# Performance work log

Measured on AMD Instinct MI355X. Metric: run time of the kernel, lower is better.

The kernel has to match this reference:

```python
import jax, jax.numpy as jnp
import numpy as np

NUM_NODES = 50000
NUM_RELATIONS = 16
NUM_EDGES = 800000
HIDDEN = 64
NUM_CLASSES = 16


def setup_inputs() -> dict:
    key = jax.random.key(0)
    ks = jax.random.split(key, 8)
    edge_index = jax.random.randint(ks[0], (2, NUM_EDGES), 0, NUM_NODES, dtype=jnp.int32)
    edge_type = jax.random.randint(ks[1], (NUM_EDGES,), 0, NUM_RELATIONS, dtype=jnp.int32)
    node_emb = jax.random.normal(ks[2], (NUM_NODES, HIDDEN), dtype=jnp.float32) * 0.1
    W1 = jax.random.normal(ks[3], (NUM_RELATIONS, HIDDEN, HIDDEN), dtype=jnp.float32) * 0.1
    root1 = jax.random.normal(ks[4], (HIDDEN, HIDDEN), dtype=jnp.float32) * 0.1
    b1 = jnp.zeros((HIDDEN,), dtype=jnp.float32)
    W2 = jax.random.normal(ks[5], (NUM_RELATIONS, HIDDEN, NUM_CLASSES), dtype=jnp.float32) * 0.1
    root2 = jax.random.normal(ks[6], (HIDDEN, NUM_CLASSES), dtype=jnp.float32) * 0.1
    b2 = jnp.zeros((NUM_CLASSES,), dtype=jnp.float32)
    return {"edge_index": edge_index, "edge_type": edge_type, "node_emb": node_emb,
            "W1": W1, "root1": root1, "b1": b1, "W2": W2, "root2": root2, "b2": b2}


def rgcn_conv(x, src, dst, edge_type, W, root, bias, num_nodes):
    # PyG RGCNConv (aggr='mean', root_weight=True, bias=True, num_bases=None):
    # per relation r: transform all nodes, gather at src, scatter-MEAN at dst
    # (mean over edges of that relation per target node); sum over relations;
    # then add root transform and bias.
    out_dim = W.shape[-1]

    def body(acc, rw):
        W_r, r = rw
        h = x @ W_r                                   # [N, out]
        mask = (edge_type == r).astype(x.dtype)       # [E]
        msg = h[src] * mask[:, None]                  # [E, out]
        summed = jax.ops.segment_sum(msg, dst, num_segments=num_nodes)  # [N, out]
        cnt = jax.ops.segment_sum(mask, dst, num_segments=num_nodes)    # [N]
        mean = jnp.where(cnt[:, None] > 0, summed / jnp.maximum(cnt, 1.0)[:, None], 0.0)
        return acc + mean, None

    acc0 = jnp.zeros((num_nodes, out_dim), dtype=x.dtype)
    agg, _ = jax.lax.scan(body, acc0, (W, jnp.arange(W.shape[0])))
    return agg + x @ root + bias


def reference(edge_index, edge_type, node_emb, W1, root1, b1, W2, root2, b2):
    src, dst = edge_index[0], edge_index[1]
    n = node_emb.shape[0]
    x = rgcn_conv(node_emb, src, dst, edge_type, W1, root1, b1, n)
    x = jax.nn.relu(x)  # dropout p=0.0 -> identity
    x = rgcn_conv(x, src, dst, edge_type, W2, root2, b2, n)
    return x
```

## Files before the change

### kernel.cpp

```cpp
#include <hip/hip_runtime.h>
#include <hip/hip_bf16.h>

#define N_NODES 50000
#define NREL 16
#define HID 64
#define NCLS 16
#define NBKT (N_NODES * NREL)
#define SB 2048
#define NSB ((NBKT + SB - 1) / SB)
#define TILE 32
#define NTB ((N_NODES + TILE - 1) / TILE)
#define XCHUNKS (N_NODES * HID / 8)
#define W1N (17 * HID * HID)
#define W2N (17 * NCLS * HID)

typedef __attribute__((ext_vector_type(8))) short bf16x8;
typedef __attribute__((ext_vector_type(4))) float f32x4;

static __device__ __forceinline__ unsigned short f2bf(float f) {
    __hip_bfloat16 h = __float2bfloat16(f);
    return *reinterpret_cast<unsigned short*>(&h);
}
static __device__ __forceinline__ float bf2f(unsigned short u) {
    __hip_bfloat16 h;
    *reinterpret_cast<unsigned short*>(&h) = u;
    return __bfloat162float(h);
}


__global__ __launch_bounds__(256) void pre_k(const int* __restrict__ dstp,
                                             const int* __restrict__ et,
                                             int* __restrict__ bcnt,
                                             int* __restrict__ rank, int E,
                                             const float* __restrict__ x,
                                             const float* __restrict__ W1,
                                             const float* __restrict__ root1,
                                             const float* __restrict__ W2,
                                             const float* __restrict__ root2,
                                             ushort* __restrict__ xb,
                                             ushort* __restrict__ WbT1,
                                             ushort* __restrict__ WbT2) {
    int eb = (E + 255) >> 8;
    if ((int)blockIdx.x < eb) {
        int i = blockIdx.x * 256 + threadIdx.x;
        if (i < E) {
            int b = dstp[i] * NREL + et[i];
            rank[i] = atomicAdd(&bcnt[b], 1);
        }
        return;
    }
    int i = (blockIdx.x - eb) * 256 + threadIdx.x;
    if (i < XCHUNKS) {
        float4 f0 = *(const float4*)(x + (size_t)i * 8);
        float4 f1 = *(const float4*)(x + (size_t)i * 8 + 4);
        bf16x8 o;
        o[0] = (short)f2bf(f0.x); o[1] = (short)f2bf(f0.y);
        o[2] = (short)f2bf(f0.z); o[3] = (short)f2bf(f0.w);
        o[4] = (short)f2bf(f1.x); o[5] = (short)f2bf(f1.y);
        o[6] = (short)f2bf(f1.z); o[7] = (short)f2bf(f1.w);
        *(bf16x8*)(xb + (size_t)i * 8) = o;
    } else {
        int j = i - XCHUNKS;
        if (j < W1N) {
            int t = j >> 12, rem = j & 4095, n = rem >> 6, k = rem & 63;
            float v = (t < 16) ? W1[(size_t)t * HID * HID + k * HID + n]
                               : root1[k * HID + n];
            WbT1[j] = f2bf(v);
        } else {
            int m = j - W1N;
            if (m < W2N) {
                int t = m >> 10, rem = m & 1023, n = rem >> 6, k = rem & 63;
                float v = (t < 16) ? W2[(size_t)t * HID * NCLS + k * NCLS + n]
                                   : root2[k * NCLS + n];
                WbT2[m] = f2bf(v);
            }
        }
    }
}

__global__ __launch_bounds__(256) void scan1_k(const int* __restrict__ bcnt,
                                               int* __restrict__ bsum) {
    int b = blockIdx.x, t = threadIdx.x;
    int base = b * SB + t * 8;
    int s = 0;
#pragma unroll
    for (int j = 0; j < 8; ++j)
        if (base + j < NBKT) s += bcnt[base + j];
#pragma unroll
    for (int off = 1; off < 64; off <<= 1) s += __shfl_xor(s, off, 64);
    __shared__ int ws[4];
    if ((t & 63) == 0) ws[t >> 6] = s;
    __syncthreads();
    if (t == 0) bsum[b] = ws[0] + ws[1] + ws[2] + ws[3];
}

__global__ __launch_bounds__(512) void scan2_k(int* __restrict__ bsum,
                                               int* __restrict__ rstart, int E) {
    __shared__ int ts[512];
    int t = threadIdx.x;
    int v = (t < NSB) ? bsum[t] : 0;
    ts[t] = v;
    __syncthreads();
    int acc = v;
    for (int off = 1; off < 512; off <<= 1) {
        int u = (t >= off) ? ts[t - off] : 0;
        __syncthreads();
        acc += u;
        ts[t] = acc;
        __syncthreads();
    }
    if (t < NSB) bsum[t] = acc - v;
    if (t == 0) rstart[NBKT] = E;
}

__global__ __launch_bounds__(256) void scan3_k(int* __restrict__ bcnt,
                                               const int* __restrict__ bsum) {
    int b = blockIdx.x, t = threadIdx.x;
    int base = b * SB + t * 8;
    int a[8];
    int s = 0;
#pragma unroll
    for (int j = 0; j < 8; ++j) {
        a[j] = (base + j < NBKT) ? bcnt[base + j] : 0;
        s += a[j];
    }
    __shared__ int ts[256];
    ts[t] = s;
    __syncthreads();
    int acc = s;
    for (int off = 1; off < 256; off <<= 1) {
        int u = (t >= off) ? ts[t - off] : 0;
        __syncthreads();
        acc += u;
        ts[t] = acc;
        __syncthreads();
    }
    int run = bsum[b] + (acc - s);
#pragma unroll
    for (int j = 0; j < 8; ++j) {
        if (base + j < NBKT) bcnt[base + j] = run;
        run += a[j];
    }
}

__global__ __launch_bounds__(256) void scat_k(const int* __restrict__ srcp,
                                              const int* __restrict__ dstp,
                                              const int* __restrict__ et,
                                              const int* __restrict__ rank,
                                              const int* __restrict__ rstart,
                                              int2* __restrict__ sedge, int E) {
    int i = blockIdx.x * 256 + threadIdx.x;
    if (i < E) {
        int r = et[i];
        int b = dstp[i] * NREL + r;
        int lo = rstart[b], hi = rstart[b + 1];
        float inv = 1.0f / (float)(hi - lo);
        sedge[lo + rank[i]] = make_int2(srcp[i] | (r << 16), __float_as_int(inv));
    }
}


#define GFLUSH()                                                              \
    {                                                                         \
        bf16x8 o_;                                                            \
        o_[0] = (short)f2bf(acc[0]); o_[1] = (short)f2bf(acc[1]);             \
        o_[2] = (short)f2bf(acc[2]); o_[3] = (short)f2bf(acc[3]);             \
        o_[4] = (short)f2bf(acc[4]); o_[5] = (short)f2bf(acc[5]);             \
        o_[6] = (short)f2bf(acc[6]); o_[7] = (short)f2bf(acc[7]);             \
        *(bf16x8*)(Ab + ((curRel * (TILE * 128) + rowoff) ^ sw)) = o_;        \
        acc[0] = 0.f; acc[1] = 0.f; acc[2] = 0.f; acc[3] = 0.f;               \
        acc[4] = 0.f; acc[5] = 0.f; acc[6] = 0.f; acc[7] = 0.f;               \
    }

static __device__ __forceinline__ void gather_tile(char* Ab,
                                                   const ushort* __restrict__ ft,
                                                   const int2* __restrict__ sedge,
                                                   const int* __restrict__ rstart,
                                                   int dst0, int tid) {
    int g = tid >> 3, l8 = tid & 7;
    int node = dst0 + g;
    bool valid = node < N_NODES;

    int lo = 0, hi = 0;
    if (valid) {
        lo = rstart[node * NREL];
        hi = rstart[node * NREL + NREL];
    }
    int deg = hi - lo;
    int base = (deg > 0) ? lo : 0;
    int last = (deg > 0) ? hi - 1 : 0;

    int sw = (g & 7) << 4;
    int rowoff = (g << 7) + (l8 << 4);
    const bf16x8 zz = {0, 0, 0, 0, 0, 0, 0, 0};

    int2 d[32];
#pragma unroll
    for (int j = 0; j < 32; ++j) {
        int idx = base + j;
        if (idx > last) idx = last;
        d[j] = sedge[idx];
    }

#pragma unroll
    for (int t = 0; t < 16; ++t)
        *(bf16x8*)(Ab + ((t * (TILE * 128) + rowoff) ^ sw)) = zz;
    {
        bf16x8 v = zz;
        if (valid) v = *(const bf16x8*)(ft + (size_t)node * HID + l8 * 8);
        *(bf16x8*)(Ab + ((16 * (TILE * 128) + rowoff) ^ sw)) = v;
    }

    const ushort* xcol = ft + l8 * 8;
    bf16x8 v[32];
#pragma unroll
    for (int j = 0; j < 32; ++j)
        v[j] = *(const bf16x8*)(xcol + (size_t)(d[j].x & 0xFFFF) * HID);
    __builtin_amdgcn_sched_barrier(0);

    float acc[8] = {0.f, 0.f, 0.f, 0.f, 0.f, 0.f, 0.f, 0.f};
    int curRel = 0;
#pragma unroll
    for (int j = 0; j < 32; ++j) {
        if (j < deg) {
            int r_ = (d[j].x >> 16) & 15;
            if (r_ != curRel) {
                GFLUSH();
                curRel = r_;
            }
            float inv_ = __int_as_float(d[j].y);
#pragma unroll
            for (int q = 0; q < 8; ++q)
                acc[q] = fmaf(inv_, bf2f((unsigned short)v[j][q]), acc[q]);
        }
    }

    for (int e = lo + 32; e < hi; ++e) {
        int2 m = sedge[e];
        int r = (m.x >> 16) & 15;
        if (r != curRel) {
            GFLUSH();
            curRel = r;
        }
        float inv = __int_as_float(m.y);
        bf16x8 vv = *(const bf16x8*)(xcol + (size_t)(m.x & 0xFFFF) * HID);
#pragma unroll
        for (int q = 0; q < 8; ++q)
            acc[q] = fmaf(inv, bf2f((unsigned short)vv[q]), acc[q]);
    }
    if (deg > 0) GFLUSH();
}

__global__ __launch_bounds__(256, 2) void fuse1_k(const ushort* __restrict__ xb,
                                                  const int2* __restrict__ sedge,
                                                  const int* __restrict__ rstart,
                                                  const ushort* __restrict__ WbT1,
                                                  const float* __restrict__ b1,
                                                  ushort* __restrict__ X1b) {
    __shared__ bf16x8 Abuf[17 * TILE * 8];
    char* Ab = (char*)Abuf;
    int tid = threadIdx.x;
    int dst0 = blockIdx.x * TILE;

    gather_tile(Ab, xb, sedge, rstart, dst0, tid);

    int wave = tid >> 6, lane = tid & 63;
    int mr = lane & 15, kq = lane >> 4;
    f32x4 c0 = {0.f, 0.f, 0.f, 0.f}, c1 = {0.f, 0.f, 0.f, 0.f};
    const ushort* wb = WbT1 + (wave * 16 + mr) * HID + kq * 8;
    int sw = (mr & 7) << 4;
    int a00o = ((mr << 7) + (kq << 4)) ^ sw;
    int a01o = ((mr << 7) + 64 + (kq << 4)) ^ sw;
    int a10o = (((16 + mr) << 7) + (kq << 4)) ^ sw;
    int a11o = (((16 + mr) << 7) + 64 + (kq << 4)) ^ sw;

    bf16x8 bk0 = *(const bf16x8*)(wb);
    bf16x8 bk1 = *(const bf16x8*)(wb + 32);
    __syncthreads();

    for (int t = 0; t < 17; ++t) {
        bf16x8 nb0 = bk0, nb1 = bk1;
        if (t < 16) {
            nb0 = *(const bf16x8*)(wb + (t + 1) * 4096);
            nb1 = *(const bf16x8*)(wb + (t + 1) * 4096 + 32);
        }
        const char* At = Ab + t * (TILE * 128);
        bf16x8 a00 = *(const bf16x8*)(At + a00o);
        bf16x8 a01 = *(const bf16x8*)(At + a01o);
        bf16x8 a10 = *(const bf16x8*)(At + a10o);
        bf16x8 a11 = *(const bf16x8*)(At + a11o);
        c0 = __builtin_amdgcn_mfma_f32_16x16x32_bf16(a00, bk0, c0, 0, 0, 0);
        c0 = __builtin_amdgcn_mfma_f32_16x16x32_bf16(a01, bk1, c0, 0, 0, 0);
        c1 = __builtin_amdgcn_mfma_f32_16x16x32_bf16(a10, bk0, c1, 0, 0, 0);
        c1 = __builtin_amdgcn_mfma_f32_16x16x32_bf16(a11, bk1, c1, 0, 0, 0);
        bk0 = nb0;
        bk1 = nb1;
    }
    float bias = b1[wave * 16 + mr];
    int col = wave * 16 + mr;
#pragma unroll
    for (int j = 0; j < 4; ++j) {
        int r0 = dst0 + kq * 4 + j;
        if (r0 < N_NODES)
            X1b[(size_t)r0 * HID + col] = f2bf(fmaxf(c0[j] + bias, 0.f));
        int r1 = r0 + 16;
        if (r1 < N_NODES)
            X1b[(size_t)r1 * HID + col] = f2bf(fmaxf(c1[j] + bias, 0.f));
    }
}

__global__ __launch_bounds__(256, 2) void fuse2_k(const ushort* __restrict__ X1b,
                                                  const int2* __restrict__ sedge,
                                                  const int* __restrict__ rstart,
                                                  const ushort* __restrict__ WbT2,
                                                  const float* __restrict__ b2,
                                                  float* __restrict__ out) {
    __shared__ bf16x8 Abuf[17 * TILE * 8];
    __shared__ float P[4 * TILE * NCLS];
    char* Ab = (char*)Abuf;
    int tid = threadIdx.x;
    int dst0 = blockIdx.x * TILE;

    gather_tile(Ab, X1b, sedge, rstart, dst0, tid);

    int wave = tid >> 6, lane = tid & 63;
    int mr = lane & 15, kq = lane >> 4;
    f32x4 c0 = {0.f, 0.f, 0.f, 0.f}, c1 = {0.f, 0.f, 0.f, 0.f};
    const ushort* wb = WbT2 + mr * HID + kq * 8;
    int sw = (mr & 7) << 4;
    int a00o = ((mr << 7) + (kq << 4)) ^ sw;
    int a01o = ((mr << 7) + 64 + (kq << 4)) ^ sw;
    int a10o = (((16 + mr) << 7) + (kq << 4)) ^ sw;
    int a11o = (((16 + mr) << 7) + 64 + (kq << 4)) ^ sw;

    bf16x8 bk0 = *(const bf16x8*)(wb + wave * 1024);
    bf16x8 bk1 = *(const bf16x8*)(wb + wave * 1024 + 32);
    __syncthreads();

    for (int t = wave; t < 17; t += 4) {
        bf16x8 nb0 = bk0, nb1 = bk1;
        if (t + 4 < 17) {
            nb0 = *(const bf16x8*)(wb + (t + 4) * 1024);
            nb1 = *(const bf16x8*)(wb + (t + 4) * 1024 + 32);
        }
        const char* At = Ab + t * (TILE * 128);
        bf16x8 a00 = *(const bf16x8*)(At + a00o);
        bf16x8 a01 = *(const bf16x8*)(At + a01o);
        bf16x8 a10 = *(const bf16x8*)(At + a10o);
        bf16x8 a11 = *(const bf16x8*)(At + a11o);
        c0 = __builtin_amdgcn_mfma_f32_16x16x32_bf16(a00, bk0, c0, 0, 0, 0);
        c0 = __builtin_amdgcn_mfma_f32_16x16x32_bf16(a01, bk1, c0, 0, 0, 0);
        c1 = __builtin_amdgcn_mfma_f32_16x16x32_bf16(a10, bk0, c1, 0, 0, 0);
        c1 = __builtin_amdgcn_mfma_f32_16x16x32_bf16(a11, bk1, c1, 0, 0, 0);
        bk0 = nb0;
        bk1 = nb1;
    }
    float* Pw = P + wave * (TILE * NCLS);
#pragma unroll
    for (int j = 0; j < 4; ++j) {
        Pw[(kq * 4 + j) * NCLS + mr] = c0[j];
        Pw[(16 + kq * 4 + j) * NCLS + mr] = c1[j];
    }
    __syncthreads();

    int idx = tid * 2;
    int row = idx >> 4, c = idx & 15;
    float s0 = P[idx] + P[512 + idx] + P[1024 + idx] + P[1536 + idx] + b2[c];
    float s1 = P[idx + 1] + P[512 + idx + 1] + P[1024 + idx + 1] +
               P[1536 + idx + 1] + b2[c + 1];
    if (dst0 + row < N_NODES) {
        float2 o = make_float2(s0, s1);
        *(float2*)(out + (size_t)(dst0 + row) * NCLS + c) = o;
    }
}

extern "C" void kernel_launch(void* const* d_in, const int* in_sizes, int n_in,
                              void* d_out, int out_size, void* d_ws, size_t ws_size,
                              hipStream_t stream) {
    const int* ei    = (const int*)d_in[0];
    const int* et    = (const int*)d_in[1];
    const float* x   = (const float*)d_in[2];
    const float* W1  = (const float*)d_in[3];
    const float* r1  = (const float*)d_in[4];
    const float* b1  = (const float*)d_in[5];
    const float* W2  = (const float*)d_in[6];
    const float* r2  = (const float*)d_in[7];
    const float* b2  = (const float*)d_in[8];
    float* out = (float*)d_out;

    int E = in_sizes[0] / 2;
    const int* srcp = ei;
    const int* dstp = ei + E;

    int*    bcnt  = (int*)d_ws;
    int*    rank  = bcnt + (NBKT + 20);
    int*    bsum  = rank + E;
    int2*   sedge = (int2*)(bsum + 512);
    ushort* WbT1  = (ushort*)(sedge + E);
    ushort* WbT2  = WbT1 + W1N;
    ushort* xb    = WbT2 + W2N;
    ushort* X1b   = xb + (size_t)N_NODES * HID;
    int*    rstart = bcnt;

    hipMemsetAsync(bcnt, 0, (NBKT + 20) * sizeof(int), stream);

    int eb = (E + 255) / 256;
    int cvtThreads = XCHUNKS + W1N + W2N;
    int cvtBlocks = (cvtThreads + 255) / 256;

    pre_k<<<eb + cvtBlocks, 256, 0, stream>>>(dstp, et, bcnt, rank, E,
                                              x, W1, r1, W2, r2, xb, WbT1, WbT2);
    scan1_k<<<NSB, 256, 0, stream>>>(bcnt, bsum);
    scan2_k<<<1, 512, 0, stream>>>(bsum, rstart, E);
    scan3_k<<<NSB, 256, 0, stream>>>(bcnt, bsum);
    scat_k<<<eb, 256, 0, stream>>>(srcp, dstp, et, rank, rstart, sedge, E);

    fuse1_k<<<NTB, 256, 0, stream>>>(xb, sedge, rstart, WbT1, b1, X1b);
    fuse2_k<<<NTB, 256, 0, stream>>>(X1b, sedge, rstart, WbT2, b2, out);
}
```

Baseline: 240.2 us.

## Shrink node tile to 16, split gather by relation halves, use cursor atomics

Halves the destination-node tile to 16 so each block has twice the gather parallelism: two 8-thread groups per node each handle half of the relations, with 16 edges prefetched each. The root (self) features are loaded straight into registers as the MFMA A operand instead of being staged in LDS, and occupancy hints go from 2 to 3 blocks per CU. Edge bucketing stops storing a per-edge rank from the counting pass and instead places edges with a second atomic cursor in the scatter pass, which adds a cursor array and a second round of atomics. Bounds checks are removed because N_NODES divides evenly by the tile, and launches double in number with less MFMA work per block.

After: 278.9 us. +16.1%, slower.

```diff
diff --git a/kernel.cpp b/kernel.cpp
--- a/kernel.cpp
+++ b/kernel.cpp
@@ -8,8 +8,8 @@
 #define NBKT (N_NODES * NREL)
 #define SB 2048
 #define NSB ((NBKT + SB - 1) / SB)
-#define TILE 32
-#define NTB ((N_NODES + TILE - 1) / TILE)
+#define TILE 16
+#define NTB (N_NODES / TILE)
 #define XCHUNKS (N_NODES * HID / 8)
 #define W1N (17 * HID * HID)
 #define W2N (17 * NCLS * HID)
@@ -30,8 +30,7 @@
 
 __global__ __launch_bounds__(256) void pre_k(const int* __restrict__ dstp,
                                              const int* __restrict__ et,
-                                             int* __restrict__ bcnt,
-                                             int* __restrict__ rank, int E,
+                                             int* __restrict__ bcnt, int E,
                                              const float* __restrict__ x,
                                              const float* __restrict__ W1,
                                              const float* __restrict__ root1,
@@ -43,10 +42,7 @@
     int eb = (E + 255) >> 8;
     if ((int)blockIdx.x < eb) {
         int i = blockIdx.x * 256 + threadIdx.x;
-        if (i < E) {
-            int b = dstp[i] * NREL + et[i];
-            rank[i] = atomicAdd(&bcnt[b], 1);
-        }
+        if (i < E) atomicAdd(&bcnt[dstp[i] * NREL + et[i]], 1);
         return;
     }
     int i = (blockIdx.x - eb) * 256 + threadIdx.x;
@@ -114,7 +110,8 @@
 }
 
 __global__ __launch_bounds__(256) void scan3_k(int* __restrict__ bcnt,
-                                               const int* __restrict__ bsum) {
+                                               const int* __restrict__ bsum,
+                                               int* __restrict__ cursor) {
     int b = blockIdx.x, t = threadIdx.x;
     int base = b * SB + t * 8;
     int a[8];
@@ -138,7 +135,10 @@
     int run = bsum[b] + (acc - s);
 #pragma unroll
     for (int j = 0; j < 8; ++j) {
-        if (base + j < NBKT) bcnt[base + j] = run;
+        if (base + j < NBKT) {
+            bcnt[base + j] = run;
+            cursor[base + j] = run;
+        }
         run += a[j];
     }
 }
@@ -146,16 +146,16 @@
 __global__ __launch_bounds__(256) void scat_k(const int* __restrict__ srcp,
                                               const int* __restrict__ dstp,
                                               const int* __restrict__ et,
-                                              const int* __restrict__ rank,
                                               const int* __restrict__ rstart,
+                                              int* __restrict__ cursor,
                                               int2* __restrict__ sedge, int E) {
     int i = blockIdx.x * 256 + threadIdx.x;
     if (i < E) {
         int r = et[i];
         int b = dstp[i] * NREL + r;
-        int lo = rstart[b], hi = rstart[b + 1];
-        float inv = 1.0f / (float)(hi - lo);
-        sedge[lo + rank[i]] = make_int2(srcp[i] | (r << 16), __float_as_int(inv));
+        int p = atomicAdd(&cursor[b], 1);
+        float inv = 1.0f / (float)(rstart[b + 1] - rstart[b]);
+        sedge[p] = make_int2(srcp[i] | (r << 16), __float_as_int(inv));
     }
 }
 
@@ -177,15 +177,11 @@
                                                    const int2* __restrict__ sedge,
                                                    const int* __restrict__ rstart,
                                                    int dst0, int tid) {
-    int g = tid >> 3, l8 = tid & 7;
+    int grp = tid >> 3, l8 = tid & 7;
+    int g = grp & 15, h = grp >> 4;
     int node = dst0 + g;
-    bool valid = node < N_NODES;
-
-    int lo = 0, hi = 0;
-    if (valid) {
-        lo = rstart[node * NREL];
-        hi = rstart[node * NREL + NREL];
-    }
+    int b0 = node * NREL + h * 8;
+    int lo = rstart[b0], hi = rstart[b0 + 8];
     int deg = hi - lo;
     int base = (deg > 0) ? lo : 0;
     int last = (deg > 0) ? hi - 1 : 0;
@@ -194,34 +190,29 @@
     int rowoff = (g << 7) + (l8 << 4);
     const bf16x8 zz = {0, 0, 0, 0, 0, 0, 0, 0};
 
-    int2 d[32];
-#pragma unroll
-    for (int j = 0; j < 32; ++j) {
+    int2 d[16];
+#pragma unroll
+    for (int j = 0; j < 16; ++j) {
         int idx = base + j;
         if (idx > last) idx = last;
         d[j] = sedge[idx];
     }
 
 #pragma unroll
-    for (int t = 0; t < 16; ++t)
-        *(bf16x8*)(Ab + ((t * (TILE * 128) + rowoff) ^ sw)) = zz;
-    {
-        bf16x8 v = zz;
-        if (valid) v = *(const bf16x8*)(ft + (size_t)node * HID + l8 * 8);
-        *(bf16x8*)(Ab + ((16 * (TILE * 128) + rowoff) ^ sw)) = v;
-    }
+    for (int r = 0; r < 8; ++r)
+        *(bf16x8*)(Ab + (((h * 8 + r) * (TILE * 128) + rowoff) ^ sw)) = zz;
 
     const ushort* xcol = ft + l8 * 8;
-    bf16x8 v[32];
-#pragma unroll
-    for (int j = 0; j < 32; ++j)
+    bf16x8 v[16];
+#pragma unroll
+    for (int j = 0; j < 16; ++j)
         v[j] = *(const bf16x8*)(xcol + (size_t)(d[j].x & 0xFFFF) * HID);
     __builtin_amdgcn_sched_barrier(0);
 
     float acc[8] = {0.f, 0.f, 0.f, 0.f, 0.f, 0.f, 0.f, 0.f};
-    int curRel = 0;
-#pragma unroll
-    for (int j = 0; j < 32; ++j) {
+    int curRel = h * 8;
+#pragma unroll
+    for (int j = 0; j < 16; ++j) {
         if (j < deg) {
             int r_ = (d[j].x >> 16) & 15;
             if (r_ != curRel) {
@@ -234,8 +225,7 @@
                 acc[q] = fmaf(inv_, bf2f((unsigned short)v[j][q]), acc[q]);
         }
     }
-
-    for (int e = lo + 32; e < hi; ++e) {
+    for (int e = lo + 16; e < hi; ++e) {
         int2 m = sedge[e];
         int r = (m.x >> 16) & 15;
         if (r != curRel) {
@@ -251,127 +241,107 @@
     if (deg > 0) GFLUSH();
 }
 
-__global__ __launch_bounds__(256, 2) void fuse1_k(const ushort* __restrict__ xb,
+__global__ __launch_bounds__(256, 3) void fuse1_k(const ushort* __restrict__ xb,
                                                   const int2* __restrict__ sedge,
                                                   const int* __restrict__ rstart,
                                                   const ushort* __restrict__ WbT1,
                                                   const float* __restrict__ b1,
                                                   ushort* __restrict__ X1b) {
-    __shared__ bf16x8 Abuf[17 * TILE * 8];
+    __shared__ bf16x8 Abuf[NREL * TILE * 8];
     char* Ab = (char*)Abuf;
     int tid = threadIdx.x;
     int dst0 = blockIdx.x * TILE;
-
-    gather_tile(Ab, xb, sedge, rstart, dst0, tid);
-
     int wave = tid >> 6, lane = tid & 63;
     int mr = lane & 15, kq = lane >> 4;
-    f32x4 c0 = {0.f, 0.f, 0.f, 0.f}, c1 = {0.f, 0.f, 0.f, 0.f};
+
+    const ushort* xrow = xb + (size_t)(dst0 + mr) * HID + kq * 8;
+    bf16x8 ra0 = *(const bf16x8*)(xrow);
+    bf16x8 ra1 = *(const bf16x8*)(xrow + 32);
+
+    gather_tile(Ab, xb, sedge, rstart, dst0, tid);
+
     const ushort* wb = WbT1 + (wave * 16 + mr) * HID + kq * 8;
     int sw = (mr & 7) << 4;
-    int a00o = ((mr << 7) + (kq << 4)) ^ sw;
-    int a01o = ((mr << 7) + 64 + (kq << 4)) ^ sw;
-    int a10o = (((16 + mr) << 7) + (kq << 4)) ^ sw;
-    int a11o = (((16 + mr) << 7) + 64 + (kq << 4)) ^ sw;
+    int a0o = ((mr << 7) + (kq << 4)) ^ sw;
+    int a1o = ((mr << 7) + 64 + (kq << 4)) ^ sw;
 
     bf16x8 bk0 = *(const bf16x8*)(wb);
     bf16x8 bk1 = *(const bf16x8*)(wb + 32);
     __syncthreads();
 
-    for (int t = 0; t < 17; ++t) {
-        bf16x8 nb0 = bk0, nb1 = bk1;
-        if (t < 16) {
-            nb0 = *(const bf16x8*)(wb + (t + 1) * 4096);
-            nb1 = *(const bf16x8*)(wb + (t + 1) * 4096 + 32);
-        }
+    f32x4 c = {0.f, 0.f, 0.f, 0.f};
+    for (int t = 0; t < 16; ++t) {
+        bf16x8 nb0 = *(const bf16x8*)(wb + (t + 1) * 4096);
+        bf16x8 nb1 = *(const bf16x8*)(wb + (t + 1) * 4096 + 32);
         const char* At = Ab + t * (TILE * 128);
-        bf16x8 a00 = *(const bf16x8*)(At + a00o);
-        bf16x8 a01 = *(const bf16x8*)(At + a01o);
-        bf16x8 a10 = *(const bf16x8*)(At + a10o);
-        bf16x8 a11 = *(const bf16x8*)(At + a11o);
-        c0 = __builtin_amdgcn_mfma_f32_16x16x32_bf16(a00, bk0, c0, 0, 0, 0);
-        c0 = __builtin_amdgcn_mfma_f32_16x16x32_bf16(a01, bk1, c0, 0, 0, 0);
-        c1 = __builtin_amdgcn_mfma_f32_16x16x32_bf16(a10, bk0, c1, 0, 0, 0);
-        c1 = __builtin_amdgcn_mfma_f32_16x16x32_bf16(a11, bk1, c1, 0, 0, 0);
+        bf16x8 a0 = *(const bf16x8*)(At + a0o);
+        bf16x8 a1 = *(const bf16x8*)(At + a1o);
+        c = __builtin_amdgcn_mfma_f32_16x16x32_bf16(a0, bk0, c, 0, 0, 0);
+        c = __builtin_amdgcn_mfma_f32_16x16x32_bf16(a1, bk1, c, 0, 0, 0);
         bk0 = nb0;
         bk1 = nb1;
     }
+    c = __builtin_amdgcn_mfma_f32_16x16x32_bf16(ra0, bk0, c, 0, 0, 0);
+    c = __builtin_amdgcn_mfma_f32_16x16x32_bf16(ra1, bk1, c, 0, 0, 0);
+
     float bias = b1[wave * 16 + mr];
     int col = wave * 16 + mr;
 #pragma unroll
     for (int j = 0; j < 4; ++j) {
-        int r0 = dst0 + kq * 4 + j;
-        if (r0 < N_NODES)
-            X1b[(size_t)r0 * HID + col] = f2bf(fmaxf(c0[j] + bias, 0.f));
-        int r1 = r0 + 16;
-        if (r1 < N_NODES)
-            X1b[(size_t)r1 * HID + col] = f2bf(fmaxf(c1[j] + bias, 0.f));
-    }
-}
-
-__global__ __launch_bounds__(256, 2) void fuse2_k(const ushort* __restrict__ X1b,
+        int node = dst0 + kq * 4 + j;
+        X1b[(size_t)node * HID + col] = f2bf(fmaxf(c[j] + bias, 0.f));
+    }
+}
+
+__global__ __launch_bounds__(256, 3) void fuse2_k(const ushort* __restrict__ X1b,
                                                   const int2* __restrict__ sedge,
                                                   const int* __restrict__ rstart,
                                                   const ushort* __restrict__ WbT2,
                                                   const float* __restrict__ b2,
                                                   float* __restrict__ out) {
-    __shared__ bf16x8 Abuf[17 * TILE * 8];
-    __shared__ float P[4 * TILE * NCLS];
+    __shared__ bf16x8 Abuf[NREL * TILE * 8];
+    __shared__ float P[4][TILE * NCLS];
     char* Ab = (char*)Abuf;
     int tid = threadIdx.x;
     int dst0 = blockIdx.x * TILE;
-
-    gather_tile(Ab, X1b, sedge, rstart, dst0, tid);
-
     int wave = tid >> 6, lane = tid & 63;
     int mr = lane & 15, kq = lane >> 4;
-    f32x4 c0 = {0.f, 0.f, 0.f, 0.f}, c1 = {0.f, 0.f, 0.f, 0.f};
+
+    const ushort* xrow = X1b + (size_t)(dst0 + mr) * HID + kq * 8;
+    bf16x8 ra0 = *(const bf16x8*)(xrow);
+    bf16x8 ra1 = *(const bf16x8*)(xrow + 32);
+
+    gather_tile(Ab, X1b, sedge, rstart, dst0, tid);
+    __syncthreads();
+
     const ushort* wb = WbT2 + mr * HID + kq * 8;
     int sw = (mr & 7) << 4;
-    int a00o = ((mr << 7) + (kq << 4)) ^ sw;
-    int a01o = ((mr << 7) + 64 + (kq << 4)) ^ sw;
-    int a10o = (((16 + mr) << 7) + (kq << 4)) ^ sw;
-    int a11o = (((16 + mr) << 7) + 64 + (kq << 4)) ^ sw;
-
-    bf16x8 bk0 = *(const bf16x8*)(wb + wave * 1024);
-    bf16x8 bk1 = *(const bf16x8*)(wb + wave * 1024 + 32);
-    __syncthreads();
-
-    for (int t = wave; t < 17; t += 4) {
-        bf16x8 nb0 = bk0, nb1 = bk1;
-        if (t + 4 < 17) {
-            nb0 = *(const bf16x8*)(wb + (t + 4) * 1024);
-            nb1 = *(const bf16x8*)(wb + (t + 4) * 1024 + 32);
-        }
+    int a0o = ((mr << 7) + (kq << 4)) ^ sw;
+    int a1o = ((mr << 7) + 64 + (kq << 4)) ^ sw;
+
+    f32x4 c = {0.f, 0.f, 0.f, 0.f};
+    for (int t = wave; t < 16; t += 4) {
+        bf16x8 bk0 = *(const bf16x8*)(wb + t * (NCLS * HID));
+        bf16x8 bk1 = *(const bf16x8*)(wb + t * (NCLS * HID) + 32);
         const char* At = Ab + t * (TILE * 128);
-        bf16x8 a00 = *(const bf16x8*)(At + a00o);
-        bf16x8 a01 = *(const bf16x8*)(At + a01o);
-        bf16x8 a10 = *(const bf16x8*)(At + a10o);
-        bf16x8 a11 = *(const bf16x8*)(At + a11o);
-        c0 = __builtin_amdgcn_mfma_f32_16x16x32_bf16(a00, bk0, c0, 0, 0, 0);
-        c0 = __builtin_amdgcn_mfma_f32_16x16x32_bf16(a01, bk1, c0, 0, 0, 0);
-        c1 = __builtin_amdgcn_mfma_f32_16x16x32_bf16(a10, bk0, c1, 0, 0, 0);
-        c1 = __builtin_amdgcn_mfma_f32_16x16x32_bf16(a11, bk1, c1, 0, 0, 0);
-        bk0 = nb0;
-        bk1 = nb1;
-    }
-    float* Pw = P + wave * (TILE * NCLS);
-#pragma unroll
-    for (int j = 0; j < 4; ++j) {
-        Pw[(kq * 4 + j) * NCLS + mr] = c0[j];
-        Pw[(16 + kq * 4 + j) * NCLS + mr] = c1[j];
-    }
-    __syncthreads();
-
-    int idx = tid * 2;
-    int row = idx >> 4, c = idx & 15;
-    float s0 = P[idx] + P[512 + idx] + P[1024 + idx] + P[1536 + idx] + b2[c];
-    float s1 = P[idx + 1] + P[512 + idx + 1] + P[1024 + idx + 1] +
-               P[1536 + idx + 1] + b2[c + 1];
-    if (dst0 + row < N_NODES) {
-        float2 o = make_float2(s0, s1);
-        *(float2*)(out + (size_t)(dst0 + row) * NCLS + c) = o;
-    }
+        bf16x8 a0 = *(const bf16x8*)(At + a0o);
+        bf16x8 a1 = *(const bf16x8*)(At + a1o);
+        c = __builtin_amdgcn_mfma_f32_16x16x32_bf16(a0, bk0, c, 0, 0, 0);
+        c = __builtin_amdgcn_mfma_f32_16x16x32_bf16(a1, bk1, c, 0, 0, 0);
+    }
+    if (wave == 0) {
+        bf16x8 bk0 = *(const bf16x8*)(wb + 16 * (NCLS * HID));
+        bf16x8 bk1 = *(const bf16x8*)(wb + 16 * (NCLS * HID) + 32);
+        c = __builtin_amdgcn_mfma_f32_16x16x32_bf16(ra0, bk0, c, 0, 0, 0);
+        c = __builtin_amdgcn_mfma_f32_16x16x32_bf16(ra1, bk1, c, 0, 0, 0);
+    }
+#pragma unroll
+    for (int j = 0; j < 4; ++j) P[wave][(kq * 4 + j) * NCLS + mr] = c[j];
+    __syncthreads();
+
+    int row = tid >> 4, cc = tid & 15;
+    float s = P[0][tid] + P[1][tid] + P[2][tid] + P[3][tid] + b2[cc];
+    out[(size_t)(dst0 + row) * NCLS + cc] = s;
 }
 
 extern "C" void kernel_launch(void* const* d_in, const int* in_sizes, int n_in,
@@ -392,14 +362,14 @@
     const int* srcp = ei;
     const int* dstp = ei + E;
 
-    int*    bcnt  = (int*)d_ws;
-    int*    rank  = bcnt + (NBKT + 20);
-    int*    bsum  = rank + E;
-    int2*   sedge = (int2*)(bsum + 512);
-    ushort* WbT1  = (ushort*)(sedge + E);
-    ushort* WbT2  = WbT1 + W1N;
-    ushort* xb    = WbT2 + W2N;
-    ushort* X1b   = xb + (size_t)N_NODES * HID;
+    int*    bcnt   = (int*)d_ws;
+    int*    cursor = bcnt + (NBKT + 20);
+    int*    bsum   = cursor + NBKT;
+    int2*   sedge  = (int2*)(bsum + 512);
+    ushort* WbT1   = (ushort*)(sedge + E);
+    ushort* WbT2   = WbT1 + W1N;
+    ushort* xb     = WbT2 + W2N;
+    ushort* X1b    = xb + (size_t)N_NODES * HID;
     int*    rstart = bcnt;
 
     hipMemsetAsync(bcnt, 0, (NBKT + 20) * sizeof(int), stream);
@@ -408,12 +378,12 @@
     int cvtThreads = XCHUNKS + W1N + W2N;
     int cvtBlocks = (cvtThreads + 255) / 256;
 
-    pre_k<<<eb + cvtBlocks, 256, 0, stream>>>(dstp, et, bcnt, rank, E,
+    pre_k<<<eb + cvtBlocks, 256, 0, stream>>>(dstp, et, bcnt, E,
                                               x, W1, r1, W2, r2, xb, WbT1, WbT2);
     scan1_k<<<NSB, 256, 0, stream>>>(bcnt, bsum);
     scan2_k<<<1, 512, 0, stream>>>(bsum, rstart, E);
-    scan3_k<<<NSB, 256, 0, stream>>>(bcnt, bsum);
-    scat_k<<<eb, 256, 0, stream>>>(srcp, dstp, et, rank, rstart, sedge, E);
+    scan3_k<<<NSB, 256, 0, stream>>>(bcnt, bsum, cursor);
+    scat_k<<<eb, 256, 0, stream>>>(srcp, dstp, et, rstart, cursor, sedge, E);
 
     fuse1_k<<<NTB, 256, 0, stream>>>(xb, sedge, rstart, WbT1, b1, X1b);
     fuse2_k<<<NTB, 256, 0, stream>>>(X1b, sedge, rstart, WbT2, b2, out);
```

## Split per-node gather across two thread groups by relation half, use 512-thread blocks

Applied to the files above, without the earlier changes.

Each destination node's edge gather is now split between two 8-lane groups, one handling relations 0-7 and the other 8-15, so a 32-node tile is served by 512 threads. The self/root row no longer goes through shared memory. It is loaded directly into registers and applied as a final MFMA step, which shrinks LDS to 16 relation slabs. Fuse1 splits output rows across wave halves, and fuse2 spreads relations over 8 waves with a two-stage LDS reduction. The aim is more memory-level parallelism in the latency-bound gather, at the cost of extra synchronisation and more blocks needed per CU.

Measured after the change: 264.6 us. +10.1%, slower.

```diff
diff --git a/kernel.cpp b/kernel.cpp
--- a/kernel.cpp
+++ b/kernel.cpp
@@ -177,14 +177,15 @@
                                                    const int2* __restrict__ sedge,
                                                    const int* __restrict__ rstart,
                                                    int dst0, int tid) {
-    int g = tid >> 3, l8 = tid & 7;
+    int grp = tid >> 3, l8 = tid & 7;
+    int g = grp & 31, h = grp >> 5;
     int node = dst0 + g;
     bool valid = node < N_NODES;
-
     int lo = 0, hi = 0;
     if (valid) {
-        lo = rstart[node * NREL];
-        hi = rstart[node * NREL + NREL];
+        int b0 = node * NREL + h * 8;
+        lo = rstart[b0];
+        hi = rstart[b0 + 8];
     }
     int deg = hi - lo;
     int base = (deg > 0) ? lo : 0;
@@ -194,34 +195,29 @@
     int rowoff = (g << 7) + (l8 << 4);
     const bf16x8 zz = {0, 0, 0, 0, 0, 0, 0, 0};
 
-    int2 d[32];
-#pragma unroll
-    for (int j = 0; j < 32; ++j) {
+    int2 d[16];
+#pragma unroll
+    for (int j = 0; j < 16; ++j) {
         int idx = base + j;
         if (idx > last) idx = last;
         d[j] = sedge[idx];
     }
 
 #pragma unroll
-    for (int t = 0; t < 16; ++t)
-        *(bf16x8*)(Ab + ((t * (TILE * 128) + rowoff) ^ sw)) = zz;
-    {
-        bf16x8 v = zz;
-        if (valid) v = *(const bf16x8*)(ft + (size_t)node * HID + l8 * 8);
-        *(bf16x8*)(Ab + ((16 * (TILE * 128) + rowoff) ^ sw)) = v;
-    }
+    for (int r = 0; r < 8; ++r)
+        *(bf16x8*)(Ab + (((h * 8 + r) * (TILE * 128) + rowoff) ^ sw)) = zz;
 
     const ushort* xcol = ft + l8 * 8;
-    bf16x8 v[32];
-#pragma unroll
-    for (int j = 0; j < 32; ++j)
+    bf16x8 v[16];
+#pragma unroll
+    for (int j = 0; j < 16; ++j)
         v[j] = *(const bf16x8*)(xcol + (size_t)(d[j].x & 0xFFFF) * HID);
     __builtin_amdgcn_sched_barrier(0);
 
     float acc[8] = {0.f, 0.f, 0.f, 0.f, 0.f, 0.f, 0.f, 0.f};
-    int curRel = 0;
-#pragma unroll
-    for (int j = 0; j < 32; ++j) {
+    int curRel = h * 8;
+#pragma unroll
+    for (int j = 0; j < 16; ++j) {
         if (j < deg) {
             int r_ = (d[j].x >> 16) & 15;
             if (r_ != curRel) {
@@ -234,8 +230,7 @@
                 acc[q] = fmaf(inv_, bf2f((unsigned short)v[j][q]), acc[q]);
         }
     }
-
-    for (int e = lo + 32; e < hi; ++e) {
+    for (int e = lo + 16; e < hi; ++e) {
         int2 m = sedge[e];
         int r = (m.x >> 16) & 15;
         if (r != curRel) {
@@ -251,39 +246,105 @@
     if (deg > 0) GFLUSH();
 }
 
-__global__ __launch_bounds__(256, 2) void fuse1_k(const ushort* __restrict__ xb,
+__global__ __launch_bounds__(512, 4) void fuse1_k(const ushort* __restrict__ xb,
                                                   const int2* __restrict__ sedge,
                                                   const int* __restrict__ rstart,
                                                   const ushort* __restrict__ WbT1,
                                                   const float* __restrict__ b1,
                                                   ushort* __restrict__ X1b) {
-    __shared__ bf16x8 Abuf[17 * TILE * 8];
+    __shared__ bf16x8 Abuf[NREL * TILE * 8];
     char* Ab = (char*)Abuf;
     int tid = threadIdx.x;
     int dst0 = blockIdx.x * TILE;
-
-    gather_tile(Ab, xb, sedge, rstart, dst0, tid);
-
     int wave = tid >> 6, lane = tid & 63;
     int mr = lane & 15, kq = lane >> 4;
-    f32x4 c0 = {0.f, 0.f, 0.f, 0.f}, c1 = {0.f, 0.f, 0.f, 0.f};
-    const ushort* wb = WbT1 + (wave * 16 + mr) * HID + kq * 8;
+    int cg = wave & 3, mh = wave >> 2;
+
+    int rnode = dst0 + mh * 16 + mr;
+    if (rnode >= N_NODES) rnode = N_NODES - 1;
+    const ushort* xrow = xb + (size_t)rnode * HID + kq * 8;
+    bf16x8 ra0 = *(const bf16x8*)(xrow);
+    bf16x8 ra1 = *(const bf16x8*)(xrow + 32);
+
+    gather_tile(Ab, xb, sedge, rstart, dst0, tid);
+
+    const ushort* wb = WbT1 + (cg * 16 + mr) * HID + kq * 8;
+    int sw = (mr & 7) << 4;
+    int arow = mh * 16 + mr;
+    int a0o = ((arow << 7) + (kq << 4)) ^ sw;
+    int a1o = ((arow << 7) + 64 + (kq << 4)) ^ sw;
+
+    bf16x8 bk0 = *(const bf16x8*)(wb);
+    bf16x8 bk1 = *(const bf16x8*)(wb + 32);
+    __syncthreads();
+
+    f32x4 c = {0.f, 0.f, 0.f, 0.f};
+    for (int t = 0; t < 16; ++t) {
+        bf16x8 nb0 = *(const bf16x8*)(wb + (t + 1) * 4096);
+        bf16x8 nb1 = *(const bf16x8*)(wb + (t + 1) * 4096 + 32);
+        const char* At = Ab + t * (TILE * 128);
+        bf16x8 a0 = *(const bf16x8*)(At + a0o);
+        bf16x8 a1 = *(const bf16x8*)(At + a1o);
+        c = __builtin_amdgcn_mfma_f32_16x16x32_bf16(a0, bk0, c, 0, 0, 0);
+        c = __builtin_amdgcn_mfma_f32_16x16x32_bf16(a1, bk1, c, 0, 0, 0);
+        bk0 = nb0;
+        bk1 = nb1;
+    }
+    c = __builtin_amdgcn_mfma_f32_16x16x32_bf16(ra0, bk0, c, 0, 0, 0);
+    c = __builtin_amdgcn_mfma_f32_16x16x32_bf16(ra1, bk1, c, 0, 0, 0);
+
+    float bias = b1[cg * 16 + mr];
+    int col = cg * 16 + mr;
+#pragma unroll
+    for (int j = 0; j < 4; ++j) {
+        int node = dst0 + mh * 16 + kq * 4 + j;
+        if (node < N_NODES)
+            X1b[(size_t)node * HID + col] = f2bf(fmaxf(c[j] + bias, 0.f));
+    }
+}
+
+__global__ __launch_bounds__(512, 4) void fuse2_k(const ushort* __restrict__ X1b,
+                                                  const int2* __restrict__ sedge,
+                                                  const int* __restrict__ rstart,
+                                                  const ushort* __restrict__ WbT2,
+                                                  const float* __restrict__ b2,
+                                                  float* __restrict__ out) {
+    __shared__ bf16x8 Abuf[NREL * TILE * 8];
+    __shared__ float P[4][TILE * NCLS];
+    char* Ab = (char*)Abuf;
+    int tid = threadIdx.x;
+    int dst0 = blockIdx.x * TILE;
+    int wave = tid >> 6, lane = tid & 63;
+    int mr = lane & 15, kq = lane >> 4;
+
+    bf16x8 ra00, ra01, ra10, ra11;
+    if (wave == 0) {
+        int r0 = dst0 + mr;
+        if (r0 >= N_NODES) r0 = N_NODES - 1;
+        int r1 = dst0 + 16 + mr;
+        if (r1 >= N_NODES) r1 = N_NODES - 1;
+        const ushort* x0 = X1b + (size_t)r0 * HID + kq * 8;
+        const ushort* x1 = X1b + (size_t)r1 * HID + kq * 8;
+        ra00 = *(const bf16x8*)(x0);
+        ra01 = *(const bf16x8*)(x0 + 32);
+        ra10 = *(const bf16x8*)(x1);
+        ra11 = *(const bf16x8*)(x1 + 32);
+    }
+
+    gather_tile(Ab, X1b, sedge, rstart, dst0, tid);
+    __syncthreads();
+
+    const ushort* wb = WbT2 + mr * HID + kq * 8;
     int sw = (mr & 7) << 4;
     int a00o = ((mr << 7) + (kq << 4)) ^ sw;
     int a01o = ((mr << 7) + 64 + (kq << 4)) ^ sw;
     int a10o = (((16 + mr) << 7) + (kq << 4)) ^ sw;
     int a11o = (((16 + mr) << 7) + 64 + (kq << 4)) ^ sw;
 
-    bf16x8 bk0 = *(const bf16x8*)(wb);
-    bf16x8 bk1 = *(const bf16x8*)(wb + 32);
-    __syncthreads();
-
-    for (int t = 0; t < 17; ++t) {
-        bf16x8 nb0 = bk0, nb1 = bk1;
-        if (t < 16) {
-            nb0 = *(const bf16x8*)(wb + (t + 1) * 4096);
-            nb1 = *(const bf16x8*)(wb + (t + 1) * 4096 + 32);
-        }
+    f32x4 c0 = {0.f, 0.f, 0.f, 0.f}, c1 = {0.f, 0.f, 0.f, 0.f};
+    for (int t = wave; t < 16; t += 8) {
+        bf16x8 bk0 = *(const bf16x8*)(wb + t * 1024);
+        bf16x8 bk1 = *(const bf16x8*)(wb + t * 1024 + 32);
         const char* At = Ab + t * (TILE * 128);
         bf16x8 a00 = *(const bf16x8*)(At + a00o);
         bf16x8 a01 = *(const bf16x8*)(At + a01o);
@@ -293,85 +354,36 @@
         c0 = __builtin_amdgcn_mfma_f32_16x16x32_bf16(a01, bk1, c0, 0, 0, 0);
         c1 = __builtin_amdgcn_mfma_f32_16x16x32_bf16(a10, bk0, c1, 0, 0, 0);
         c1 = __builtin_amdgcn_mfma_f32_16x16x32_bf16(a11, bk1, c1, 0, 0, 0);
-        bk0 = nb0;
-        bk1 = nb1;
-    }
-    float bias = b1[wave * 16 + mr];
-    int col = wave * 16 + mr;
-#pragma unroll
-    for (int j = 0; j < 4; ++j) {
-        int r0 = dst0 + kq * 4 + j;
-        if (r0 < N_NODES)
-            X1b[(size_t)r0 * HID + col] = f2bf(fmaxf(c0[j] + bias, 0.f));
-        int r1 = r0 + 16;
-        if (r1 < N_NODES)
-            X1b[(size_t)r1 * HID + col] = f2bf(fmaxf(c1[j] + bias, 0.f));
-    }
-}
-
-__global__ __launch_bounds__(256, 2) void fuse2_k(const ushort* __restrict__ X1b,
-                                                  const int2* __restrict__ sedge,
-                                                  const int* __restrict__ rstart,
-                                                  const ushort* __restrict__ WbT2,
-                                                  const float* __restrict__ b2,
-                                                  float* __restrict__ out) {
-    __shared__ bf16x8 Abuf[17 * TILE * 8];
-    __shared__ float P[4 * TILE * NCLS];
-    char* Ab = (char*)Abuf;
-    int tid = threadIdx.x;
-    int dst0 = blockIdx.x * TILE;
-
-    gather_tile(Ab, X1b, sedge, rstart, dst0, tid);
-
-    int wave = tid >> 6, lane = tid & 63;
-    int mr = lane & 15, kq = lane >> 4;
-    f32x4 c0 = {0.f, 0.f, 0.f, 0.f}, c1 = {0.f, 0.f, 0.f, 0.f};
-    const ushort* wb = WbT2 + mr * HID + kq * 8;
-    int sw = (mr & 7) << 4;
-    int a00o = ((mr << 7) + (kq << 4)) ^ sw;
-    int a01o = ((mr << 7) + 64 + (kq << 4)) ^ sw;
-    int a10o = (((16 + mr) << 7) + (kq << 4)) ^ sw;
-    int a11o = (((16 + mr) << 7) + 64 + (kq << 4)) ^ sw;
-
-    bf16x8 bk0 = *(const bf16x8*)(wb + wave * 1024);
-    bf16x8 bk1 = *(const bf16x8*)(wb + wave * 1024 + 32);
-    __syncthreads();
-
-    for (int t = wave; t < 17; t += 4) {
-        bf16x8 nb0 = bk0, nb1 = bk1;
-        if (t + 4 < 17) {
-            nb0 = *(const bf16x8*)(wb + (t + 4) * 1024);
-            nb1 = *(const bf16x8*)(wb + (t + 4) * 1024 + 32);
-        }
-        const char* At = Ab + t * (TILE * 128);
-        bf16x8 a00 = *(const bf16x8*)(At + a00o);
-        bf16x8 a01 = *(const bf16x8*)(At + a01o);
-        bf16x8 a10 = *(const bf16x8*)(At + a10o);
-        bf16x8 a11 = *(const bf16x8*)(At + a11o);
-        c0 = __builtin_amdgcn_mfma_f32_16x16x32_bf16(a00, bk0, c0, 0, 0, 0);
-        c0 = __builtin_amdgcn_mfma_f32_16x16x32_bf16(a01, bk1, c0, 0, 0, 0);
-        c1 = __builtin_amdgcn_mfma_f32_16x16x32_bf16(a10, bk0, c1, 0, 0, 0);
-        c1 = __builtin_amdgcn_mfma_f32_16x16x32_bf16(a11, bk1, c1, 0, 0, 0);
-        bk0 = nb0;
-        bk1 = nb1;
-    }
-    float* Pw = P + wave * (TILE * NCLS);
-#pragma unroll
-    for (int j = 0; j < 4; ++j) {
-        Pw[(kq * 4 + j) * NCLS + mr] = c0[j];
-        Pw[(16 + kq * 4 + j) * NCLS + mr] = c1[j];
-    }
-    __syncthreads();
-
-    int idx = tid * 2;
-    int row = idx >> 4, c = idx & 15;
-    float s0 = P[idx] + P[512 + idx] + P[1024 + idx] + P[1536 + idx] + b2[c];
-    float s1 = P[idx + 1] + P[512 + idx + 1] + P[1024 + idx + 1] +
-               P[1536 + idx + 1] + b2[c + 1];
-    if (dst0 + row < N_NODES) {
-        float2 o = make_float2(s0, s1);
-        *(float2*)(out + (size_t)(dst0 + row) * NCLS + c) = o;
-    }
+    }
+    if (wave == 0) {
+        bf16x8 bk0 = *(const bf16x8*)(wb + 16 * 1024);
+        bf16x8 bk1 = *(const bf16x8*)(wb + 16 * 1024 + 32);
+        c0 = __builtin_amdgcn_mfma_f32_16x16x32_bf16(ra00, bk0, c0, 0, 0, 0);
+        c0 = __builtin_amdgcn_mfma_f32_16x16x32_bf16(ra01, bk1, c0, 0, 0, 0);
+        c1 = __builtin_amdgcn_mfma_f32_16x16x32_bf16(ra10, bk0, c1, 0, 0, 0);
+        c1 = __builtin_amdgcn_mfma_f32_16x16x32_bf16(ra11, bk1, c1, 0, 0, 0);
+    }
+
+    if (wave < 4) {
+#pragma unroll
+        for (int j = 0; j < 4; ++j) {
+            P[wave][(kq * 4 + j) * NCLS + mr] = c0[j];
+            P[wave][(16 + kq * 4 + j) * NCLS + mr] = c1[j];
+        }
+    }
+    __syncthreads();
+    if (wave >= 4) {
+#pragma unroll
+        for (int j = 0; j < 4; ++j) {
+            P[wave - 4][(kq * 4 + j) * NCLS + mr] += c0[j];
+            P[wave - 4][(16 + kq * 4 + j) * NCLS + mr] += c1[j];
+        }
+    }
+    __syncthreads();
+
+    int row = tid >> 4, cc = tid & 15;
+    float s = P[0][tid] + P[1][tid] + P[2][tid] + P[3][tid] + b2[cc];
+    if (dst0 + row < N_NODES) out[(size_t)(dst0 + row) * NCLS + cc] = s;
 }
 
 extern "C" void kernel_launch(void* const* d_in, const int* in_sizes, int n_in,
@@ -415,6 +427,6 @@
     scan3_k<<<NSB, 256, 0, stream>>>(bcnt, bsum);
     scat_k<<<eb, 256, 0, stream>>>(srcp, dstp, et, rank, rstart, sedge, E);
 
-    fuse1_k<<<NTB, 256, 0, stream>>>(xb, sedge, rstart, WbT1, b1, X1b);
-    fuse2_k<<<NTB, 256, 0, stream>>>(X1b, sedge, rstart, WbT2, b2, out);
-}
+    fuse1_k<<<NTB, 512, 0, stream>>>(xb, sedge, rstart, WbT1, b1, X1b);
+    fuse2_k<<<NTB, 512, 0, stream>>>(X1b, sedge, rstart, WbT2, b2, out);
+}
```
